# Kernel optimization log

Measured on AMD Instinct MI355X. Metric: run time of the kernel, lower is better.

## Reference

```python
import jax, jax.numpy as jnp
import numpy as np

B, S, D, K = 128, 200, 128, 4
NQ, NC = 10000, 500


def setup_inputs() -> dict:
    key = jax.random.key(0)
    ks = jax.random.split(key, 20)
    f = jnp.float32
    inp = {}
    inp["question_seq"] = jax.random.randint(ks[0], (B, S), 0, NQ)
    inp["hint_attempt_seq"] = jax.random.randint(ks[1], (B, S), 0, 12)
    inp["correct_seq"] = jax.random.randint(ks[2], (B, S), 0, 2)
    inp["interval_time_seq"] = jax.random.randint(ks[3], (B, S), 0, 100)
    inp["use_time_seq"] = jax.random.randint(ks[4], (B, S), 0, 100)
    inp["q2c_table"] = jax.random.randint(ks[5], (NQ, K), 0, NC)
    inp["q2c_mask_table"] = jax.random.randint(ks[6], (NQ, K), 0, 2)
    s = 0.1
    inp["embed_question"] = jax.random.normal(ks[7], (NQ, D), f) * s
    inp["embed_question_disc"] = jax.random.normal(ks[8], (NQ, 1), f) * s
    inp["embed_concept"] = jax.random.normal(ks[9], (NC, D), f) * s
    inp["embed_interval_time"] = jax.random.normal(ks[10], (100, D), f) * s
    inp["embed_use_time"] = jax.random.normal(ks[11], (100, D), f) * s
    inp["embed_hint_attempt"] = jax.random.normal(ks[12], (12, D), f) * s
    inp["W_fuse"] = jax.random.normal(ks[13], (2 * D, D), f) / np.float32(np.sqrt(2 * D))
    inp["b_fuse"] = jnp.zeros((D,), f)
    inp["W_absorb"] = jax.random.normal(ks[14], (3 * D, D), f) / np.float32(np.sqrt(3 * D))
    inp["b_absorb"] = jnp.zeros((D,), f)
    inp["W_forget"] = jax.random.normal(ks[15], (3 * D, D), f) / np.float32(np.sqrt(3 * D))
    inp["b_forget"] = jnp.zeros((D,), f)
    inp["latent0"] = jax.random.normal(ks[16], (B, D), f) * 0.1  # xavier-init latent_pre
    return inp


def _cos(a, b, eps=1e-8):
    # torch.cosine_similarity semantics with eps clamp on each norm
    num = jnp.sum(a * b, axis=-1)
    na = jnp.sqrt(jnp.sum(a * a, axis=-1))
    nb = jnp.sqrt(jnp.sum(b * b, axis=-1))
    return num / (jnp.maximum(na, eps) * jnp.maximum(nb, eps))


def _forward(question_seq, hint_attempt_seq, correct_seq, interval_time_seq, use_time_seq,
             q2c_table, q2c_mask_table,
             embed_question, embed_question_disc, embed_concept, embed_interval_time,
             embed_use_time, embed_hint_attempt,
             W_fuse, b_fuse, W_absorb, b_absorb, W_forget, b_forget, latent0):
    f = latent0.dtype
    qe = embed_question[question_seq]                                # [B,S,D]
    qd = jax.nn.sigmoid(embed_question_disc[question_seq]) * 10.0    # [B,S,1]
    ce = jnp.broadcast_to(correct_seq.astype(f)[:, :, None], qe.shape)  # [B,S,D]
    ite = embed_interval_time[interval_time_seq]                     # [B,S,D]
    ute = embed_use_time[use_time_seq]                               # [B,S,D]
    hae = embed_hint_attempt[hint_attempt_seq]                       # [B,S,D]
    cp = embed_concept[q2c_table[question_seq]]                      # [B,S,K,D]
    m = q2c_mask_table[question_seq].astype(f)                       # [B,S,K]

    tm = lambda x: jnp.swapaxes(x, 0, 1)  # time-major for scan
    xs = (tm(qe[:, :-1]), tm(ce[:, :-1]), tm(ute[:, :-1]), tm(hae[:, :-1]), tm(ite[:, :-1]),
          tm(cp[:, :-1]), tm(cp[:, 1:]), tm(qd[:, 1:]), tm(m[:, :-1]))

    def step(lp, x):
        qe_t, ce_t, ute_t, hae_t, ite_t, cp_t, cp_t1, qd_t1, m_t = x
        inter = jnp.concatenate([qe_t, ce_t], axis=-1) @ W_fuse + b_fuse
        absorb = jnp.concatenate([inter, ute_t, hae_t], axis=-1) @ W_absorb + b_absorb
        forget = jax.nn.sigmoid(jnp.concatenate([lp, ite_t, inter], axis=-1) @ W_forget + b_forget)
        lc = lp * forget + absorb  # dropout p=0 -> identity
        qdiff = (_cos(qe_t[:, None, :], cp_t) + 1.0) * 0.5   # [B,K]
        uab = (_cos(lc[:, None, :], cp_t1) + 1.0) * 0.5      # [B,K]
        logit = qd_t1[:, 0] * jnp.sum((uab - qdiff) * m_t, axis=-1)  # [B]
        return lc, jax.nn.sigmoid(logit)

    _, ys = jax.lax.scan(step, latent0, xs)  # ys: [S-1, B]
    y = jnp.concatenate([ys.T, jnp.zeros((latent0.shape[0], 1), f)], axis=1)  # [B,S], last col 0
    return y


def reference(question_seq, hint_attempt_seq, correct_seq, interval_time_seq, use_time_seq,
              q2c_table, q2c_mask_table,
              embed_question, embed_question_disc, embed_concept, embed_interval_time,
              embed_use_time, embed_hint_attempt,
              W_fuse, b_fuse, W_absorb, b_absorb, W_forget, b_forget, latent0):
    return _forward(question_seq, hint_attempt_seq, correct_seq, interval_time_seq, use_time_seq,
                    q2c_table, q2c_mask_table,
                    embed_question, embed_question_disc, embed_concept, embed_interval_time,
                    embed_use_time, embed_hint_attempt,
                    W_fuse, b_fuse, W_absorb, b_absorb, W_forget, b_forget, latent0)
```

## Files before the change

### kernel.cpp

```cpp
#include <hip/hip_runtime.h>
#include <hip/hip_bf16.h>

typedef unsigned short u16;

#define Bb  128
#define Ss  200
#define Tt  199
#define NQq 10000
#define NCc 500
#define CHK 16
#define NCH 13

__device__ inline float bf2f(u16 u) {
    union { unsigned int i; float f; } x;
    x.i = ((unsigned int)u) << 16;
    return x.f;
}

__device__ inline float ldf(const void* p, int i, int m) {
    if (m) return ((const float*)p)[i];
    return bf2f(((const u16*)p)[i]);
}

__device__ inline void stf(void* p, int i, int m, float v) {
    if (m) ((float*)p)[i] = v;
    else ((__hip_bfloat16*)p)[i] = __float2bfloat16(v);
}

__device__ inline int clampi(int v, int lo, int hi) {
    return v < lo ? lo : (v > hi ? hi : v);
}

__device__ inline float wave_red(float v) {
#pragma unroll
    for (int m = 32; m >= 1; m >>= 1) v += __shfl_xor(v, m);
    return v;
}

__device__ inline float4 f4add(float4 a, float4 b) {
    return make_float4(a.x + b.x, a.y + b.y, a.z + b.z, a.w + b.w);
}
__device__ inline float4 f4fma(float s, float4 a, float4 b) {
    return make_float4(fmaf(s, a.x, b.x), fmaf(s, a.y, b.y),
                       fmaf(s, a.z, b.z), fmaf(s, a.w, b.w));
}

__device__ inline int detect_mode(const void* Eq) {
    const u16* q = (const u16*)Eq;
    const int l = threadIdx.x & 63;
    float mx = 0.f;
#pragma unroll
    for (int k = 0; k < 4; ++k) {
        float a = fabsf(bf2f(q[l * 4 + k]));
        if (!(a == a)) a = 3.0e38f;
        mx = fmaxf(mx, a);
    }
#pragma unroll
    for (int s = 32; s >= 1; s >>= 1) mx = fmaxf(mx, __shfl_xor(mx, s));
    return (mx > 1.0e6f) ? 1 : 0;
}

__device__ inline void load_tile_4096(float* dst, const void* src, int base,
                                      int tid, int m) {
    if (m) {
        const float4* s = (const float4*)((const float*)src + base);
        float4* d = (float4*)dst;
#pragma unroll
        for (int k = 0; k < 4; ++k) d[tid + k * 256] = s[tid + k * 256];
    } else {
        const u16* s = (const u16*)src + base;
#pragma unroll
        for (int k = 0; k < 4; ++k) {
            const int idx = (tid + k * 256) * 4;
            uint2 v = *(const uint2*)(s + idx);
            float* d = dst + idx;
            d[0] = bf2f((u16)(v.x & 0xffff)); d[1] = bf2f((u16)(v.x >> 16));
            d[2] = bf2f((u16)(v.y & 0xffff)); d[3] = bf2f((u16)(v.y >> 16));
        }
    }
}

__global__ __launch_bounds__(256) void k_prep(
    const void* Eq, const void* Eqd, const void* Wf, const void* Wa, const void* Wg,
    const void* bfu, const void* ba, const void* bg,
    const void* Eut, const void* Eha, const void* Eit, const void* Ec,
    const int* q2c, const int* q2cm,
    float* vA0, float* vA1, float* vF0, float* vF1,
    float* PA_ut, float* PA_ha, float* PF_it, float* qdm, float* qd10,
    float* PA_q, float* PF_q) {
    const int m = detect_mode(Eq);
    const int job = blockIdx.x, tid = threadIdx.x;
    __shared__ __align__(16) float smem[12416];
    if (job < 313) {
        float* t32s = smem;
        float* At   = smem + 4224;
        float* BtW  = smem + 5376;
        float* Bt0  = smem + 4224;
        float* Bt1  = smem + 8320;
        const int r0 = job * 32;
        const int tx = tid & 15, ty = tid >> 4;
        float accT[2][8];
#pragma unroll
        for (int j = 0; j < 2; ++j)
#pragma unroll
            for (int i = 0; i < 8; ++i) accT[j][i] = 0.f;
        for (int ks = 0; ks < 4; ++ks) {
            {
                const int row = tid >> 3, seg = tid & 7;
                const int q = clampi(r0 + row, 0, NQq - 1);
                const int ei = q * 128 + ks * 32 + seg * 4;
                float* dst = At + row * 36 + seg * 4;
                if (m) {
                    float4 v = *(const float4*)((const float*)Eq + ei);
                    dst[0] = v.x; dst[1] = v.y; dst[2] = v.z; dst[3] = v.w;
                } else {
                    uint2 v = *(const uint2*)((const u16*)Eq + ei);
                    dst[0] = bf2f((u16)(v.x & 0xffff)); dst[1] = bf2f((u16)(v.x >> 16));
                    dst[2] = bf2f((u16)(v.y & 0xffff)); dst[3] = bf2f((u16)(v.y >> 16));
                }
            }
            load_tile_4096(BtW, Wf, ks * 32 * 128, tid, m);
            __syncthreads();
#pragma unroll
            for (int kk = 0; kk < 32; kk += 4) {
                float a_[2][4];
                *(float4*)&a_[0][0] = *(const float4*)(At + (ty * 2 + 0) * 36 + kk);
                *(float4*)&a_[1][0] = *(const float4*)(At + (ty * 2 + 1) * 36 + kk);
#pragma unroll
                for (int q4 = 0; q4 < 4; ++q4) {
                    float4 b0 = *(const float4*)(BtW + (kk + q4) * 128 + tx * 8);
                    float4 b1 = *(const float4*)(BtW + (kk + q4) * 128 + tx * 8 + 4);
#pragma unroll
                    for (int j = 0; j < 2; ++j) {
                        const float av = a_[j][q4];
                        accT[j][0] += av * b0.x; accT[j][1] += av * b0.y;
                        accT[j][2] += av * b0.z; accT[j][3] += av * b0.w;
                        accT[j][4] += av * b1.x; accT[j][5] += av * b1.y;
                        accT[j][6] += av * b1.z; accT[j][7] += av * b1.w;
                    }
                }
            }
            __syncthreads();
        }
#pragma unroll
        for (int j = 0; j < 2; ++j) {
            const int row = ty * 2 + j;
            *(float4*)(t32s + row * 132 + tx * 8) =
                make_float4(accT[j][0], accT[j][1], accT[j][2], accT[j][3]);
            *(float4*)(t32s + row * 132 + tx * 8 + 4) =
                make_float4(accT[j][4], accT[j][5], accT[j][6], accT[j][7]);
        }
        __syncthreads();
        float acc0[2][8], acc1[2][8];
#pragma unroll
        for (int j = 0; j < 2; ++j)
#pragma unroll
            for (int i = 0; i < 8; ++i) { acc0[j][i] = 0.f; acc1[j][i] = 0.f; }
        for (int ks2 = 0; ks2 < 4; ++ks2) {
            load_tile_4096(Bt0, Wa, ks2 * 32 * 128, tid, m);
            load_tile_4096(Bt1, Wg, 256 * 128 + ks2 * 32 * 128, tid, m);
            __syncthreads();
#pragma unroll
            for (int kk = 0; kk < 32; kk += 4) {
                float a_[2][4];
                *(float4*)&a_[0][0] =
                    *(const float4*)(t32s + (ty * 2 + 0) * 132 + ks2 * 32 + kk);
                *(float4*)&a_[1][0] =
                    *(const float4*)(t32s + (ty * 2 + 1) * 132 + ks2 * 32 + kk);
#pragma unroll
                for (int q4 = 0; q4 < 4; ++q4) {
                    float4 b0 = *(const float4*)(Bt0 + (kk + q4) * 128 + tx * 8);
                    float4 b1 = *(const float4*)(Bt0 + (kk + q4) * 128 + tx * 8 + 4);
                    float4 c0 = *(const float4*)(Bt1 + (kk + q4) * 128 + tx * 8);
                    float4 c1 = *(const float4*)(Bt1 + (kk + q4) * 128 + tx * 8 + 4);
#pragma unroll
                    for (int j = 0; j < 2; ++j) {
                        const float av = a_[j][q4];
                        acc0[j][0] += av * b0.x; acc0[j][1] += av * b0.y;
                        acc0[j][2] += av * b0.z; acc0[j][3] += av * b0.w;
                        acc0[j][4] += av * b1.x; acc0[j][5] += av * b1.y;
                        acc0[j][6] += av * b1.z; acc0[j][7] += av * b1.w;
                        acc1[j][0] += av * c0.x; acc1[j][1] += av * c0.y;
                        acc1[j][2] += av * c0.z; acc1[j][3] += av * c0.w;
                        acc1[j][4] += av * c1.x; acc1[j][5] += av * c1.y;
                        acc1[j][6] += av * c1.z; acc1[j][7] += av * c1.w;
                    }
                }
            }
            __syncthreads();
        }
#pragma unroll
        for (int j = 0; j < 2; ++j) {
            const int q = r0 + ty * 2 + j;
            if (q < NQq) {
                float* oa = PA_q + q * 128 + tx * 8;
                float* of = PF_q + q * 128 + tx * 8;
#pragma unroll
                for (int i = 0; i < 8; ++i) { oa[i] = acc0[j][i]; of[i] = acc1[j][i]; }
            }
        }
    } else if (job == 313) {
        const int col = tid & 127;
        if (tid < 128) {
            float s = 0.f;
            for (int r2 = 0; r2 < 128; ++r2) s += ldf(Wf, (128 + r2) * 128 + col, m);
            smem[col] = s;
        }
        __syncthreads();
        float a0 = 0.f, a1 = 0.f;
        if (tid < 128) {
            for (int j = 0; j < 128; ++j) {
                const float wv = ldf(Wa, j * 128 + col, m);
                a0 += ldf(bfu, j, m) * wv;
                a1 += smem[j] * wv;
            }
            vA0[col] = a0 + ldf(ba, col, m);
            vA1[col] = a1;
        } else {
            for (int j = 0; j < 128; ++j) {
                const float wv = ldf(Wg, (256 + j) * 128 + col, m);
                a0 += ldf(bfu, j, m) * wv;
                a1 += smem[j] * wv;
            }
            vF0[col] = a0 + ldf(bg, col, m);
            vF1[col] = a1;
        }
    } else if (job < 414) {
        const int r = job - 314, col = tid & 127;
        float acc = 0.f;
        if (tid < 128) {
            for (int j = 0; j < 128; ++j)
                acc += ldf(Eut, r * 128 + j, m) * ldf(Wa, (128 + j) * 128 + col, m);
            PA_ut[r * 128 + col] = acc;
        } else {
            for (int j = 0; j < 128; ++j)
                acc += ldf(Eit, r * 128 + j, m) * ldf(Wg, (128 + j) * 128 + col, m);
            PF_it[r * 128 + col] = acc;
        }
    } else if (job < 426) {
        const int r = job - 414;
        if (tid < 128) {
            float acc = 0.f;
            for (int j = 0; j < 128; ++j)
                acc += ldf(Eha, r * 128 + j, m) * ldf(Wa, (256 + j) * 128 + tid, m);
            PA_ha[r * 128 + tid] = acc;
        }
    } else {
        const int wv = tid >> 6, lane = tid & 63;
        const int q = (job - 426) * 4 + wv;
        const float qa = ldf(Eq, q * 128 + lane, m);
        const float qb = ldf(Eq, q * 128 + 64 + lane, m);
        const float nqc = fmaxf(sqrtf(wave_red(qa * qa + qb * qb)), 1e-8f);
        const int4 cc = ((const int4*)q2c)[q];
        const int4 mm = ((const int4*)q2cm)[q];
        const int cks[4] = {clampi(cc.x, 0, NCc - 1), clampi(cc.y, 0, NCc - 1),
                            clampi(cc.z, 0, NCc - 1), clampi(cc.w, 0, NCc - 1)};
        const int ms[4]  = {mm.x, mm.y, mm.z, mm.w};
        float qs = 0.f;
#pragma unroll
        for (int k = 0; k < 4; ++k) {
            const int ck = cks[k];
            const float ea = ldf(Ec, ck * 128 + lane, m);
            const float eb = ldf(Ec, ck * 128 + 64 + lane, m);
            const float dot = wave_red(qa * ea + qb * eb);
            const float nn = fmaxf(sqrtf(wave_red(ea * ea + eb * eb)), 1e-8f);
            qs += (float)ms[k] * (0.5f * dot / (nqc * nn) + 0.5f);
        }
        if (lane == 0) {
            qdm[q] = qs;
            qd10[q] = 10.f / (1.f + __expf(-ldf(Eqd, q, m)));
        }
    }
}

__global__ __launch_bounds__(256) void p4_scan(
    const int* q_seq, const int* ut_seq, const int* ha_seq, const int* it_seq,
    const int* c_seq,
    const void* Eq, const void* Wg, const void* L0,
    const float* PA_q, const float* PA_ut, const float* PA_ha,
    const float* PF_q, const float* PF_it,
    const float* vA0, const float* vA1, const float* vF0, const float* vF1,
    float* lc_seq) {
    const int m = detect_mode(Eq);
    const int b = blockIdx.x;
    const int tid = threadIdx.x;
    const int wv = tid >> 6, l = tid & 63;
    const int d0 = 2 * l;
    const int ib = wv << 5;
    const int dd = ib + (l & 31);

    __shared__ float part[2][4][128];
    __shared__ float st_ab[CHK * 128];
    __shared__ float st_pf[CHK * 128];

    float wA[32], wB[32];
#pragma unroll
    for (int k = 0; k < 32; ++k) {
        wA[k] = ldf(Wg, (ib + k) * 128 + d0, m);
        wB[k] = ldf(Wg, (ib + k) * 128 + d0 + 1, m);
    }
    float lc = (l < 32) ? ldf(L0, b * 128 + dd, m) : 0.f;

    const int srow = tid >> 4, seg = tid & 15;
    const int off8 = seg * 8;
    const float4 A0a = *(const float4*)(vA0 + off8), A0b = *(const float4*)(vA0 + off8 + 4);
    const float4 A1a = *(const float4*)(vA1 + off8), A1b = *(const float4*)(vA1 + off8 + 4);
    const float4 F0a = *(const float4*)(vF0 + off8), F0b = *(const float4*)(vF0 + off8 + 4);
    const float4 F1a = *(const float4*)(vF1 + off8), F1b = *(const float4*)(vF1 + off8 + 4);

    float4 qa0, qa1, ua0, ua1, ga0, ga1, qf0, qf1, if0, if1;
    float cf;
#define LOAD_CHUNK(C)                                                          \
    {                                                                          \
        int tt = (C) * CHK + srow; if (tt > Tt - 1) tt = Tt - 1;               \
        const int base = b * Ss + tt;                                          \
        const int qt = clampi(q_seq[base], 0, NQq - 1);                        \
        const int ut = clampi(ut_seq[base], 0, 99);                            \
        const int ha = clampi(ha_seq[base], 0, 11);                            \
        const int it = clampi(it_seq[base], 0, 99);                            \
        cf = (float)c_seq[base];                                               \
        const float* pq = PA_q + qt * 128 + off8;                              \
        qa0 = *(const float4*)pq; qa1 = *(const float4*)(pq + 4);              \
        const float* pu = PA_ut + ut * 128 + off8;                             \
        ua0 = *(const float4*)pu; ua1 = *(const float4*)(pu + 4);              \
        const float* ph = PA_ha + ha * 128 + off8;                             \
        ga0 = *(const float4*)ph; ga1 = *(const float4*)(ph + 4);              \
        const float* pf = PF_q + qt * 128 + off8;                              \
        qf0 = *(const float4*)pf; qf1 = *(const float4*)(pf + 4);              \
        const float* pi = PF_it + it * 128 + off8;                             \
        if0 = *(const float4*)pi; if1 = *(const float4*)(pi + 4);              \
    }

    LOAD_CHUNK(0)
    float lcbuf[CHK];
    int par = 0;

    for (int c = 0; c < NCH; ++c) {
        __syncthreads();
        {
            float4 ab0 = f4fma(cf, A1a, f4add(f4add(qa0, ua0), f4add(ga0, A0a)));
            float4 ab1 = f4fma(cf, A1b, f4add(f4add(qa1, ua1), f4add(ga1, A0b)));
            float4 pf0 = f4fma(cf, F1a, f4add(qf0, f4add(if0, F0a)));
            float4 pf1 = f4fma(cf, F1b, f4add(qf1, f4add(if1, F0b)));
            float4* sa = (float4*)(st_ab + srow * 128 + off8);
            sa[0] = ab0; sa[1] = ab1;
            float4* sp = (float4*)(st_pf + srow * 128 + off8);
            sp[0] = pf0; sp[1] = pf1;
        }
        if (c + 1 < NCH) LOAD_CHUNK(c + 1)
        __syncthreads();

#pragma unroll
        for (int s = 0; s < CHK; ++s) {
            float pa = 0.f, pb = 0.f;
#pragma unroll
            for (int k = 0; k < 32; ++k) {
                const float u = __uint_as_float(
                    __builtin_amdgcn_readlane(__float_as_uint(lc), k));
                pa = fmaf(u, wA[k], pa);
                pb = fmaf(u, wB[k], pb);
            }
            *(float2*)&part[par][wv][d0] = make_float2(pa, pb);
            __syncthreads();
            if (l < 32) {
                const float fs = part[par][0][dd] + part[par][1][dd]
                               + part[par][2][dd] + part[par][3][dd];
                const float ab = st_ab[(s << 7) + dd];
                const float pf = st_pf[(s << 7) + dd];
                const float fg = 1.f / (1.f + __expf(-(fs + pf)));
                lc = lc * fg + ab;
                lcbuf[s] = lc;
            }
            par ^= 1;
        }
        if (l < 32) {
#pragma unroll
            for (int s = 0; s < CHK; ++s) {
                const int t = c * CHK + s;
                if (t < Tt)
                    lc_seq[((long)t * 128 + b) * 128 + dd] = lcbuf[s];
            }
        }
    }
#undef LOAD_CHUNK
}

__global__ __launch_bounds__(256) void p5_out(
    const int* q_seq, const int* q2c, const int* q2cm,
    const float* lc_seq, const float* qdm, const float* qd10,
    const void* Eq, const void* Ec, void* out) {
    const int m = detect_mode(Eq);
    const int wv = threadIdx.x >> 6, lane = threadIdx.x & 63;
    const int r = blockIdx.x * 4 + wv;
    const int t = r >> 7, b = r & 127;
    const int qt  = clampi(q_seq[b * Ss + t], 0, NQq - 1);
    const int qt1 = clampi(q_seq[b * Ss + t + 1], 0, NQq - 1);
    const int4 mm = ((const int4*)q2cm)[qt];
    int4 ci = ((const int4*)q2c)[qt1];
    const int c0 = clampi(ci.x, 0, NCc - 1), c1 = clampi(ci.y, 0, NCc - 1);
    const int c2 = clampi(ci.z, 0, NCc - 1), c3 = clampi(ci.w, 0, NCc - 1);
    const float la = lc_seq[(long)r * 128 + lane];
    const float lb = lc_seq[(long)r * 128 + 64 + lane];
    const float e0a = ldf(Ec, c0 * 128 + lane, m), e0b = ldf(Ec, c0 * 128 + 64 + lane, m);
    const float e1a = ldf(Ec, c1 * 128 + lane, m), e1b = ldf(Ec, c1 * 128 + 64 + lane, m);
    const float e2a = ldf(Ec, c2 * 128 + lane, m), e2b = ldf(Ec, c2 * 128 + 64 + lane, m);
    const float e3a = ldf(Ec, c3 * 128 + lane, m), e3b = ldf(Ec, c3 * 128 + 64 + lane, m);
    float nl = la * la + lb * lb;
    float d0 = la * e0a + lb * e0b, n0 = e0a * e0a + e0b * e0b;
    float d1 = la * e1a + lb * e1b, n1 = e1a * e1a + e1b * e1b;
    float d2 = la * e2a + lb * e2b, n2 = e2a * e2a + e2b * e2b;
    float d3 = la * e3a + lb * e3b, n3 = e3a * e3a + e3b * e3b;
#pragma unroll
    for (int s = 32; s >= 1; s >>= 1) {
        nl += __shfl_xor(nl, s);
        d0 += __shfl_xor(d0, s); d1 += __shfl_xor(d1, s);
        d2 += __shfl_xor(d2, s); d3 += __shfl_xor(d3, s);
        n0 += __shfl_xor(n0, s); n1 += __shfl_xor(n1, s);
        n2 += __shfl_xor(n2, s); n3 += __shfl_xor(n3, s);
    }
    if (lane == 0) {
        const float inl = 1.f / fmaxf(sqrtf(nl), 1e-8f);
        const float accv =
              (float)mm.x * (0.5f * d0 * inl / fmaxf(sqrtf(n0), 1e-8f) + 0.5f)
            + (float)mm.y * (0.5f * d1 * inl / fmaxf(sqrtf(n1), 1e-8f) + 0.5f)
            + (float)mm.z * (0.5f * d2 * inl / fmaxf(sqrtf(n2), 1e-8f) + 0.5f)
            + (float)mm.w * (0.5f * d3 * inl / fmaxf(sqrtf(n3), 1e-8f) + 0.5f);
        const float logit = qd10[qt1] * (accv - qdm[qt]);
        stf(out, b * Ss + t, m, 1.f / (1.f + __expf(-logit)));
        if (t == 0) stf(out, b * Ss + 199, m, 0.f);
    }
}

extern "C" void kernel_launch(void* const* d_in, const int* in_sizes, int n_in,
                              void* d_out, int out_size, void* d_ws, size_t ws_size,
                              hipStream_t stream) {
    (void)in_sizes; (void)n_in; (void)out_size; (void)ws_size;
    const int* q_seq  = (const int*)d_in[0];
    const int* ha_seq = (const int*)d_in[1];
    const int* c_seq  = (const int*)d_in[2];
    const int* it_seq = (const int*)d_in[3];
    const int* ut_seq = (const int*)d_in[4];
    const int* q2c    = (const int*)d_in[5];
    const int* q2cm   = (const int*)d_in[6];
    const void* Eq   = d_in[7];
    const void* Eqd  = d_in[8];
    const void* Ec   = d_in[9];
    const void* Eit  = d_in[10];
    const void* Eut  = d_in[11];
    const void* Eha  = d_in[12];
    const void* Wf   = d_in[13];
    const void* bfu  = d_in[14];
    const void* Wa   = d_in[15];
    const void* ba   = d_in[16];
    const void* Wg   = d_in[17];
    const void* bg   = d_in[18];
    const void* L0   = d_in[19];

    float* ws    = (float*)d_ws;
    float* vA0   = ws;
    float* vA1   = vA0 + 128;
    float* vF0   = vA1 + 128;
    float* vF1   = vF0 + 128;
    float* PA_ut = vF1 + 128;
    float* PA_ha = PA_ut + 12800;
    float* PF_it = PA_ha + 1536;
    float* qdm   = PF_it + 12800;
    float* qd10  = qdm + 10016;
    float* PA_q  = qd10 + 10016;
    float* PF_q  = PA_q + 1280000;
    float* lc_seq= PF_q + 1280000;

    hipLaunchKernelGGL(k_prep, dim3(2926), dim3(256), 0, stream,
                       Eq, Eqd, Wf, Wa, Wg, bfu, ba, bg, Eut, Eha, Eit, Ec,
                       q2c, q2cm, vA0, vA1, vF0, vF1,
                       PA_ut, PA_ha, PF_it, qdm, qd10, PA_q, PF_q);
    hipLaunchKernelGGL(p4_scan, dim3(Bb), dim3(256), 0, stream,
                       q_seq, ut_seq, ha_seq, it_seq, c_seq, Eq, Wg, L0,
                       PA_q, PA_ut, PA_ha, PF_q, PF_it,
                       vA0, vA1, vF0, vF1, lc_seq);
    hipLaunchKernelGGL(p5_out, dim3(Tt * Bb / 4), dim3(256), 0, stream,
                       q_seq, q2c, q2cm, lc_seq, qdm, qd10, Eq, Ec, d_out);
}
```

Before: 230.2 us.

## Fuse output kernel into scan kernel, computing predictions per chunk from shared memory

Removes the separate output kernel and the global lc_seq buffer. After each scan chunk, the latent states are staged in shared memory (reusing st_ab), and the four waves compute the cosine-based predictions and write outputs directly. This saves a kernel launch and the write/read of a large intermediate. The cost is extra serial work with gather latency inside the 128-block scan, plus a possible hazard in reusing the staging buffer.

Measured after the change: 293.0 us. 1.27x slower.

```diff
diff --git a/kernel.cpp b/kernel.cpp
--- a/kernel.cpp
+++ b/kernel.cpp
@@ -273,14 +273,14 @@
     }
 }
 
-__global__ __launch_bounds__(256) void p4_scan(
+__global__ __launch_bounds__(256) void k_scan(
     const int* q_seq, const int* ut_seq, const int* ha_seq, const int* it_seq,
-    const int* c_seq,
-    const void* Eq, const void* Wg, const void* L0,
+    const int* c_seq, const int* q2c, const int* q2cm,
+    const void* Eq, const void* Ec, const void* Wg, const void* L0,
     const float* PA_q, const float* PA_ut, const float* PA_ha,
     const float* PF_q, const float* PF_it,
     const float* vA0, const float* vA1, const float* vF0, const float* vF1,
-    float* lc_seq) {
+    const float* qdm, const float* qd10, void* out) {
     const int m = detect_mode(Eq);
     const int b = blockIdx.x;
     const int tid = threadIdx.x;
@@ -375,60 +375,52 @@
         }
         if (l < 32) {
 #pragma unroll
-            for (int s = 0; s < CHK; ++s) {
-                const int t = c * CHK + s;
-                if (t < Tt)
-                    lc_seq[((long)t * 128 + b) * 128 + dd] = lcbuf[s];
+            for (int s = 0; s < CHK; ++s)
+                st_ab[(s << 7) + dd] = lcbuf[s];
+        }
+        __syncthreads();
+        for (int s = wv; s < CHK; s += 4) {
+            const int t = c * CHK + s;
+            if (t >= Tt) break;
+            const int qt  = clampi(q_seq[b * Ss + t], 0, NQq - 1);
+            const int qt1 = clampi(q_seq[b * Ss + t + 1], 0, NQq - 1);
+            const int4 mm = ((const int4*)q2cm)[qt];
+            int4 ci = ((const int4*)q2c)[qt1];
+            const int c0 = clampi(ci.x, 0, NCc - 1), c1 = clampi(ci.y, 0, NCc - 1);
+            const int c2 = clampi(ci.z, 0, NCc - 1), c3 = clampi(ci.w, 0, NCc - 1);
+            const float la = st_ab[(s << 7) + l];
+            const float lb = st_ab[(s << 7) + 64 + l];
+            const float e0a = ldf(Ec, c0 * 128 + l, m), e0b = ldf(Ec, c0 * 128 + 64 + l, m);
+            const float e1a = ldf(Ec, c1 * 128 + l, m), e1b = ldf(Ec, c1 * 128 + 64 + l, m);
+            const float e2a = ldf(Ec, c2 * 128 + l, m), e2b = ldf(Ec, c2 * 128 + 64 + l, m);
+            const float e3a = ldf(Ec, c3 * 128 + l, m), e3b = ldf(Ec, c3 * 128 + 64 + l, m);
+            float nl = la * la + lb * lb;
+            float d0_ = la * e0a + lb * e0b, n0 = e0a * e0a + e0b * e0b;
+            float d1_ = la * e1a + lb * e1b, n1 = e1a * e1a + e1b * e1b;
+            float d2_ = la * e2a + lb * e2b, n2 = e2a * e2a + e2b * e2b;
+            float d3_ = la * e3a + lb * e3b, n3 = e3a * e3a + e3b * e3b;
+#pragma unroll
+            for (int sh = 32; sh >= 1; sh >>= 1) {
+                nl  += __shfl_xor(nl, sh);
+                d0_ += __shfl_xor(d0_, sh); d1_ += __shfl_xor(d1_, sh);
+                d2_ += __shfl_xor(d2_, sh); d3_ += __shfl_xor(d3_, sh);
+                n0  += __shfl_xor(n0, sh);  n1  += __shfl_xor(n1, sh);
+                n2  += __shfl_xor(n2, sh);  n3  += __shfl_xor(n3, sh);
+            }
+            if (l == 0) {
+                const float inl = 1.f / fmaxf(sqrtf(nl), 1e-8f);
+                const float accv =
+                      (float)mm.x * (0.5f * d0_ * inl / fmaxf(sqrtf(n0), 1e-8f) + 0.5f)
+                    + (float)mm.y * (0.5f * d1_ * inl / fmaxf(sqrtf(n1), 1e-8f) + 0.5f)
+                    + (float)mm.z * (0.5f * d2_ * inl / fmaxf(sqrtf(n2), 1e-8f) + 0.5f)
+                    + (float)mm.w * (0.5f * d3_ * inl / fmaxf(sqrtf(n3), 1e-8f) + 0.5f);
+                const float logit = qd10[qt1] * (accv - qdm[qt]);
+                stf(out, b * Ss + t, m, 1.f / (1.f + __expf(-logit)));
             }
         }
     }
 #undef LOAD_CHUNK
-}
-
-__global__ __launch_bounds__(256) void p5_out(
-    const int* q_seq, const int* q2c, const int* q2cm,
-    const float* lc_seq, const float* qdm, const float* qd10,
-    const void* Eq, const void* Ec, void* out) {
-    const int m = detect_mode(Eq);
-    const int wv = threadIdx.x >> 6, lane = threadIdx.x & 63;
-    const int r = blockIdx.x * 4 + wv;
-    const int t = r >> 7, b = r & 127;
-    const int qt  = clampi(q_seq[b * Ss + t], 0, NQq - 1);
-    const int qt1 = clampi(q_seq[b * Ss + t + 1], 0, NQq - 1);
-    const int4 mm = ((const int4*)q2cm)[qt];
-    int4 ci = ((const int4*)q2c)[qt1];
-    const int c0 = clampi(ci.x, 0, NCc - 1), c1 = clampi(ci.y, 0, NCc - 1);
-    const int c2 = clampi(ci.z, 0, NCc - 1), c3 = clampi(ci.w, 0, NCc - 1);
-    const float la = lc_seq[(long)r * 128 + lane];
-    const float lb = lc_seq[(long)r * 128 + 64 + lane];
-    const float e0a = ldf(Ec, c0 * 128 + lane, m), e0b = ldf(Ec, c0 * 128 + 64 + lane, m);
-    const float e1a = ldf(Ec, c1 * 128 + lane, m), e1b = ldf(Ec, c1 * 128 + 64 + lane, m);
-    const float e2a = ldf(Ec, c2 * 128 + lane, m), e2b = ldf(Ec, c2 * 128 + 64 + lane, m);
-    const float e3a = ldf(Ec, c3 * 128 + lane, m), e3b = ldf(Ec, c3 * 128 + 64 + lane, m);
-    float nl = la * la + lb * lb;
-    float d0 = la * e0a + lb * e0b, n0 = e0a * e0a + e0b * e0b;
-    float d1 = la * e1a + lb * e1b, n1 = e1a * e1a + e1b * e1b;
-    float d2 = la * e2a + lb * e2b, n2 = e2a * e2a + e2b * e2b;
-    float d3 = la * e3a + lb * e3b, n3 = e3a * e3a + e3b * e3b;
-#pragma unroll
-    for (int s = 32; s >= 1; s >>= 1) {
-        nl += __shfl_xor(nl, s);
-        d0 += __shfl_xor(d0, s); d1 += __shfl_xor(d1, s);
-        d2 += __shfl_xor(d2, s); d3 += __shfl_xor(d3, s);
-        n0 += __shfl_xor(n0, s); n1 += __shfl_xor(n1, s);
-        n2 += __shfl_xor(n2, s); n3 += __shfl_xor(n3, s);
-    }
-    if (lane == 0) {
-        const float inl = 1.f / fmaxf(sqrtf(nl), 1e-8f);
-        const float accv =
-              (float)mm.x * (0.5f * d0 * inl / fmaxf(sqrtf(n0), 1e-8f) + 0.5f)
-            + (float)mm.y * (0.5f * d1 * inl / fmaxf(sqrtf(n1), 1e-8f) + 0.5f)
-            + (float)mm.z * (0.5f * d2 * inl / fmaxf(sqrtf(n2), 1e-8f) + 0.5f)
-            + (float)mm.w * (0.5f * d3 * inl / fmaxf(sqrtf(n3), 1e-8f) + 0.5f);
-        const float logit = qd10[qt1] * (accv - qdm[qt]);
-        stf(out, b * Ss + t, m, 1.f / (1.f + __expf(-logit)));
-        if (t == 0) stf(out, b * Ss + 199, m, 0.f);
-    }
+    if (tid == 0) stf(out, b * Ss + 199, m, 0.f);
 }
 
 extern "C" void kernel_launch(void* const* d_in, const int* in_sizes, int n_in,
@@ -468,16 +460,14 @@
     float* qd10  = qdm + 10016;
     float* PA_q  = qd10 + 10016;
     float* PF_q  = PA_q + 1280000;
-    float* lc_seq= PF_q + 1280000;
 
     hipLaunchKernelGGL(k_prep, dim3(2926), dim3(256), 0, stream,
                        Eq, Eqd, Wf, Wa, Wg, bfu, ba, bg, Eut, Eha, Eit, Ec,
                        q2c, q2cm, vA0, vA1, vF0, vF1,
                        PA_ut, PA_ha, PF_it, qdm, qd10, PA_q, PF_q);
-    hipLaunchKernelGGL(p4_scan, dim3(Bb), dim3(256), 0, stream,
-                       q_seq, ut_seq, ha_seq, it_seq, c_seq, Eq, Wg, L0,
+    hipLaunchKernelGGL(k_scan, dim3(Bb), dim3(256), 0, stream,
+                       q_seq, ut_seq, ha_seq, it_seq, c_seq, q2c, q2cm,
+                       Eq, Ec, Wg, L0,
                        PA_q, PA_ut, PA_ha, PF_q, PF_it,
-                       vA0, vA1, vF0, vF1, lc_seq);
-    hipLaunchKernelGGL(p5_out, dim3(Tt * Bb / 4), dim3(256), 0, stream,
-                       q_seq, q2c, q2cm, lc_seq, qdm, qd10, Eq, Ec, d_out);
-}
+                       vA0, vA1, vF0, vF1, qdm, qd10, d_out);
+}
```
